# Kernel tuning notes

Hardware: AMD Instinct MI355X
Metric: run time of the kernel (lower is better)

## Reference

```python
import jax, jax.numpy as jnp
import numpy as np


def setup_inputs() -> dict:
    key = jax.random.key(0)
    k1, k2 = jax.random.split(key)
    pred = jax.random.normal(k1, (4, 8192, 3), dtype=jnp.float32)
    target = jax.random.normal(k2, (4, 8192, 3), dtype=jnp.float32)
    return {"pred": pred, "target": target}


def reference(pred, target):
    # Squared pairwise distances: ||p||^2 + ||q||^2 - 2 p.q  -> (B, N1, N2)
    p2 = jnp.sum(pred * pred, axis=-1)          # (B, N1)
    q2 = jnp.sum(target * target, axis=-1)      # (B, N2)
    pq = jnp.einsum('bnd,bmd->bnm', pred, target)  # (B, N1, N2)
    d2 = jnp.maximum(p2[:, :, None] + q2[:, None, :] - 2.0 * pq, 0.0)
    forward_dist = jnp.min(d2, axis=2).mean(axis=1)   # (B,)
    backward_dist = jnp.min(d2, axis=1).mean(axis=1)  # (B,)
    chamfer = forward_dist + backward_dist
    return chamfer.mean()  # reduction='mean'
```

## Files before the change

### kernel.cpp

```cpp
#include <hip/hip_runtime.h>


typedef float f32x2 __attribute__((ext_vector_type(2)));

#define NPTS   8192
#define BATCH  4
#define RPT    8
#define BLOCK  256
#define PTILE  (RPT * BLOCK)
#define NTILES (NPTS / PTILE)
#define CHUNK  128
#define NPAIR  (CHUNK / 2)
#define NCHUNK (NPTS / CHUNK)
#define NMINS  (2 * BATCH * NPTS)

__global__ __launch_bounds__(BLOCK, 4) void chamfer_pairs(
    const float* __restrict__ pred, const float* __restrict__ target,
    int* __restrict__ mins)
{
    __shared__ f32x2 qx2[NPAIR], qy2[NPAIR], qz2[NPAIR], qw2[NPAIR];
    __shared__ int   cmin_s[CHUNK];

    const int b = blockIdx.z;
    const float* __restrict__ P = pred   + b * NPTS * 3;
    const float* __restrict__ Q = target + b * NPTS * 3;

    const int tid = threadIdx.x;
    const int i0  = blockIdx.x * PTILE + tid;
    const int j0  = blockIdx.y * CHUNK;

    if (tid < CHUNK) {
        const float* qp = Q + 3 * (j0 + tid);
        const float qx = qp[0], qy = qp[1], qz = qp[2];
        ((float*)qx2)[tid] = qx;
        ((float*)qy2)[tid] = qy;
        ((float*)qz2)[tid] = qz;
        ((float*)qw2)[tid] = fmaf(qx, qx, fmaf(qy, qy, qz * qz));
        cmin_s[tid] = 0x7F7F7F7F;
    }
    __syncthreads();

    f32x2 pxn2[RPT], pyn2[RPT], pzn2[RPT], p22[RPT];
    float m[RPT];
#pragma unroll
    for (int r = 0; r < RPT; ++r) {
        const float* pp = P + 3 * (i0 + r * BLOCK);
        const float x = pp[0], y = pp[1], z = pp[2];
        const float nx = -2.0f * x, ny = -2.0f * y, nz = -2.0f * z;
        const float p2 = fmaf(x, x, fmaf(y, y, z * z));
        pxn2[r] = (f32x2){nx, nx};
        pyn2[r] = (f32x2){ny, ny};
        pzn2[r] = (f32x2){nz, nz};
        p22[r]  = (f32x2){p2, p2};
        m[r]    = 3.0e38f;
    }

    const int soff = (tid & 63) + ((tid >> 6) << 4);

#pragma unroll 2
    for (int jj = 0; jj < NPAIR; ++jj) {
        const int jp = (soff + jj) & (NPAIR - 1);
        const f32x2 qx = qx2[jp];
        const f32x2 qy = qy2[jp];
        const f32x2 qz = qz2[jp];
        const f32x2 qw = qw2[jp];

        f32x2 d[RPT];
#pragma unroll
        for (int r = 0; r < RPT; ++r) {
            f32x2 t = __builtin_elementwise_fma(pxn2[r], qx, qw);
            t = __builtin_elementwise_fma(pyn2[r], qy, t);
            t = __builtin_elementwise_fma(pzn2[r], qz, t);
            m[r] = fminf(fminf(m[r], t.x), t.y);
            d[r] = t + p22[r];
        }
        const float cl = fminf(
            fminf(fminf(fminf(d[0].x, d[1].x), d[2].x),
                  fminf(fminf(d[3].x, d[4].x), d[5].x)),
            fminf(d[6].x, d[7].x));
        const float ch = fminf(
            fminf(fminf(fminf(d[0].y, d[1].y), d[2].y),
                  fminf(fminf(d[3].y, d[4].y), d[5].y)),
            fminf(d[6].y, d[7].y));
        atomicMin(&cmin_s[2 * jp],     __float_as_int(cl));
        atomicMin(&cmin_s[2 * jp + 1], __float_as_int(ch));
    }

    int* __restrict__ fwd = mins + b * NPTS;
    int* __restrict__ bwd = mins + (BATCH + b) * NPTS;
#pragma unroll
    for (int r = 0; r < RPT; ++r) {
        const float v = fmaxf(m[r] + p22[r].x, 0.0f);
        atomicMin(&fwd[i0 + r * BLOCK], __float_as_int(v));
    }
    __syncthreads();
    if (tid < CHUNK)
        atomicMin(&bwd[j0 + tid], cmin_s[tid]);
}

__global__ __launch_bounds__(256) void chamfer_reduce1(
    const int* __restrict__ mins, float* __restrict__ partials)
{
    __shared__ float part[4];
    const int base = blockIdx.x * 1024 + threadIdx.x;

    float s = fmaxf(__int_as_float(mins[base]),       0.0f) +
              fmaxf(__int_as_float(mins[base + 256]), 0.0f) +
              fmaxf(__int_as_float(mins[base + 512]), 0.0f) +
              fmaxf(__int_as_float(mins[base + 768]), 0.0f);

    for (int off = 32; off > 0; off >>= 1)
        s += __shfl_down(s, off, 64);
    if ((threadIdx.x & 63) == 0)
        part[threadIdx.x >> 6] = s;
    __syncthreads();

    if (threadIdx.x == 0)
        partials[blockIdx.x] = part[0] + part[1] + part[2] + part[3];
}

__global__ __launch_bounds__(64) void chamfer_reduce2(
    const float* __restrict__ partials, float* __restrict__ out)
{
    float t = partials[threadIdx.x];
    for (int off = 32; off > 0; off >>= 1)
        t += __shfl_down(t, off, 64);
    if (threadIdx.x == 0)
        out[0] = t * (1.0f / (float)(BATCH * NPTS));
}

extern "C" void kernel_launch(void* const* d_in, const int* in_sizes, int n_in,
                              void* d_out, int out_size, void* d_ws, size_t ws_size,
                              hipStream_t stream)
{
    const float* pred   = (const float*)d_in[0];
    const float* target = (const float*)d_in[1];
    float* out = (float*)d_out;
    int*   mins     = (int*)d_ws;
    float* partials = (float*)d_ws + NMINS;

    hipMemsetAsync(mins, 0x7F, (size_t)NMINS * sizeof(int), stream);

    dim3 grid(NTILES, NCHUNK, BATCH);
    chamfer_pairs<<<grid, BLOCK, 0, stream>>>(pred, target, mins);
    chamfer_reduce1<<<64, 256, 0, stream>>>(mins, partials);
    chamfer_reduce2<<<1, 64, 0, stream>>>(partials, out);
}
```

Baseline: 90.21 us.

## Replace global atomicMin with per-chunk partial minima reduced in second kernel

The pair kernel now writes per-chunk forward minima and per-tile backward minima to separate workspace buffers with plain stores instead of global atomicMin. The reduce kernel takes the min over chunks and tiles before summing. This removes the memset and the global atomics, at the cost of about 8.5 MB of extra workspace traffic read by a small reduction grid.

```diff
diff --git a/kernel.cpp b/kernel.cpp
--- a/kernel.cpp
+++ b/kernel.cpp
@@ -12,22 +12,25 @@
 #define CHUNK  128
 #define NPAIR  (CHUNK / 2)
 #define NCHUNK (NPTS / CHUNK)
-#define NMINS  (2 * BATCH * NPTS)
+#define FWDP_N (BATCH * NCHUNK * NPTS)
+#define BWDP_N (BATCH * NTILES * NPTS)
 
 __global__ __launch_bounds__(BLOCK, 4) void chamfer_pairs(
     const float* __restrict__ pred, const float* __restrict__ target,
-    int* __restrict__ mins)
+    float* __restrict__ fwd_part, float* __restrict__ bwd_part)
 {
     __shared__ f32x2 qx2[NPAIR], qy2[NPAIR], qz2[NPAIR], qw2[NPAIR];
     __shared__ int   cmin_s[CHUNK];
 
-    const int b = blockIdx.z;
+    const int b    = blockIdx.z;
+    const int tile = blockIdx.x;
+    const int chnk = blockIdx.y;
     const float* __restrict__ P = pred   + b * NPTS * 3;
     const float* __restrict__ Q = target + b * NPTS * 3;
 
     const int tid = threadIdx.x;
-    const int i0  = blockIdx.x * PTILE + tid;
-    const int j0  = blockIdx.y * CHUNK;
+    const int i0  = tile * PTILE + tid;
+    const int j0  = chnk * CHUNK;
 
     if (tid < CHUNK) {
         const float* qp = Q + 3 * (j0 + tid);
@@ -86,28 +89,44 @@
         atomicMin(&cmin_s[2 * jp + 1], __float_as_int(ch));
     }
 
-    int* __restrict__ fwd = mins + b * NPTS;
-    int* __restrict__ bwd = mins + (BATCH + b) * NPTS;
+    float* __restrict__ fp = fwd_part + ((size_t)(b * NCHUNK + chnk)) * NPTS;
 #pragma unroll
-    for (int r = 0; r < RPT; ++r) {
-        const float v = fmaxf(m[r] + p22[r].x, 0.0f);
-        atomicMin(&fwd[i0 + r * BLOCK], __float_as_int(v));
-    }
+    for (int r = 0; r < RPT; ++r)
+        fp[i0 + r * BLOCK] = fmaxf(m[r] + p22[r].x, 0.0f);
+
     __syncthreads();
     if (tid < CHUNK)
-        atomicMin(&bwd[j0 + tid], cmin_s[tid]);
+        bwd_part[((size_t)(b * NTILES + tile)) * NPTS + j0 + tid] =
+            fmaxf(__int_as_float(cmin_s[tid]), 0.0f);
 }
 
 __global__ __launch_bounds__(256) void chamfer_reduce1(
-    const int* __restrict__ mins, float* __restrict__ partials)
+    const float* __restrict__ fwd_part, const float* __restrict__ bwd_part,
+    float* __restrict__ partials)
 {
     __shared__ float part[4];
-    const int base = blockIdx.x * 1024 + threadIdx.x;
+    float s = 0.0f;
 
-    float s = fmaxf(__int_as_float(mins[base]),       0.0f) +
-              fmaxf(__int_as_float(mins[base + 256]), 0.0f) +
-              fmaxf(__int_as_float(mins[base + 512]), 0.0f) +
-              fmaxf(__int_as_float(mins[base + 768]), 0.0f);
+#pragma unroll
+    for (int t = 0; t < 2; ++t) {
+        const int gi = blockIdx.x * 512 + t * 256 + threadIdx.x;
+        const int b  = gi >> 13;
+        const int i  = gi & (NPTS - 1);
+
+        float mf = 3.0e38f;
+        const float* fp = fwd_part + ((size_t)b * NCHUNK) * NPTS + i;
+#pragma unroll 8
+        for (int c = 0; c < NCHUNK; ++c)
+            mf = fminf(mf, fp[(size_t)c * NPTS]);
+        s += mf;
+
+        float mb = 3.0e38f;
+        const float* bp = bwd_part + ((size_t)b * NTILES) * NPTS + i;
+#pragma unroll
+        for (int c = 0; c < NTILES; ++c)
+            mb = fminf(mb, bp[(size_t)c * NPTS]);
+        s += mb;
+    }
 
     for (int off = 32; off > 0; off >>= 1)
         s += __shfl_down(s, off, 64);
@@ -136,13 +155,12 @@
     const float* pred   = (const float*)d_in[0];
     const float* target = (const float*)d_in[1];
     float* out = (float*)d_out;
-    int*   mins     = (int*)d_ws;
-    float* partials = (float*)d_ws + NMINS;
-
-    hipMemsetAsync(mins, 0x7F, (size_t)NMINS * sizeof(int), stream);
+    float* fwd_part = (float*)d_ws;
+    float* bwd_part = fwd_part + FWDP_N;
+    float* partials = bwd_part + BWDP_N;
 
     dim3 grid(NTILES, NCHUNK, BATCH);
-    chamfer_pairs<<<grid, BLOCK, 0, stream>>>(pred, target, mins);
-    chamfer_reduce1<<<64, 256, 0, stream>>>(mins, partials);
+    chamfer_pairs<<<grid, BLOCK, 0, stream>>>(pred, target, fwd_part, bwd_part);
+    chamfer_reduce1<<<64, 256, 0, stream>>>(fwd_part, bwd_part, partials);
     chamfer_reduce2<<<1, 64, 0, stream>>>(partials, out);
 }
```

New measurement: 112.5 us. 24.7% more time.
